# Optimization experiments

Hardware: AMD Instinct MI355X
Metric: run time of the kernel (lower is better)

The kernel has to match this reference:

```python
import jax, jax.numpy as jnp
import numpy as np

N = 100_000      # nodes
E = 800_000      # edges (avg degree 8)
IN = 64          # in_channels
OUT = 64         # out_channels
HEADS = 4
HD = OUT // HEADS  # per-head out channels (concat=True)


def _unif(key, shape, fan_in):
    b = 1.0 / np.sqrt(fan_in)
    return jax.random.uniform(key, shape, jnp.float32, -b, b)


def setup_inputs() -> dict:
    key = jax.random.key(0)
    ks = jax.random.split(key, 12)
    x = jax.random.normal(ks[0], (N, IN), jnp.float32)
    pos = jax.random.normal(ks[1], (N, 3), jnp.float32)
    edge_index = jax.random.randint(ks[2], (2, E), 0, N, jnp.int32)
    # Per-head PointTransformerConv params (stacked over heads).
    # lin / lin_src / lin_dst are bias-free Linear(in, hd); pos_nn is Linear(3, hd) with bias.
    W_lin = _unif(ks[3], (HEADS, IN, HD), IN)
    W_src = _unif(ks[4], (HEADS, IN, HD), IN)
    W_dst = _unif(ks[5], (HEADS, IN, HD), IN)
    W_pos = _unif(ks[6], (HEADS, 3, HD), 3)
    b_pos = _unif(ks[7], (HEADS, HD), 3)
    # projection MLP: Linear(OUT,OUT) -> ReLU -> Linear(OUT,OUT)
    W1 = _unif(ks[8], (OUT, OUT), OUT)
    b1 = _unif(ks[9], (OUT,), OUT)
    W2 = _unif(ks[10], (OUT, OUT), OUT)
    b2 = _unif(ks[11], (OUT,), OUT)
    return dict(x=x, pos=pos, edge_index=edge_index, W_lin=W_lin, W_src=W_src,
                W_dst=W_dst, W_pos=W_pos, b_pos=b_pos, W1=W1, b1=b1, W2=W2, b2=b2)


def reference(x, pos, edge_index, W_lin, W_src, W_dst, W_pos, b_pos, W1, b1, W2, b2):
    # Add self-loops (PointTransformerConv default add_self_loops=True).
    loops = jnp.arange(N, dtype=edge_index.dtype)
    src = jnp.concatenate([edge_index[0], loops])   # j (source)
    dst = jnp.concatenate([edge_index[1], loops])   # i (target)

    # Per-node, all-heads projections: [N, H, HD]
    v = jnp.einsum('ni,hio->nho', x, W_lin)
    a_src = jnp.einsum('ni,hio->nho', x, W_src)
    a_dst = jnp.einsum('ni,hio->nho', x, W_dst)

    # Relative-position encoding delta = pos_nn(pos_i - pos_j): [Et, H, HD]
    rel = pos[dst] - pos[src]
    delta = jnp.einsum('ec,hco->eho', rel, W_pos) + b_pos

    # Attention logits per edge/channel: alpha_i - alpha_j + delta
    alpha = a_dst[dst] - a_src[src] + delta

    # Segment softmax over incoming edges of each target node (numerically stable).
    amax = jax.ops.segment_max(alpha, dst, num_segments=N)
    amax = jnp.where(jnp.isfinite(amax), amax, 0.0)
    ex = jnp.exp(alpha - amax[dst])
    denom = jax.ops.segment_sum(ex, dst, num_segments=N)
    attn = ex / jnp.maximum(denom[dst], 1e-16)

    # Message = attn * (lin(x_j) + delta), scatter-sum to targets: [N, H, HD]
    msg = attn * (v[src] + delta)
    out_h = jax.ops.segment_sum(msg, dst, num_segments=N)

    # Concat heads -> projection MLP
    out = out_h.reshape(N, HEADS * HD)
    h = jax.nn.relu(out @ W1 + b1)
    return h @ W2 + b2
```

## Files before the change

### kernel.cpp

```cpp
#include <hip/hip_runtime.h>
#include <math.h>


typedef _Float16 f16;
typedef _Float16 f16x2 __attribute__((ext_vector_type(2)));
typedef _Float16 f16x4 __attribute__((ext_vector_type(4)));
typedef _Float16 f16x8 __attribute__((ext_vector_type(8)));
typedef float f32x4 __attribute__((ext_vector_type(4)));

#define A_PITCH 104
#define C_PITCH 200
#define LOG2E 1.44269504f
#define S_CAP 32

__global__ __launch_bounds__(256) void zero_wprep_kernel(
    int Zb, int* __restrict__ cnt, int N,
    const float* __restrict__ Ws, const float* __restrict__ Wl,
    const float* __restrict__ Wp, const float* __restrict__ bp,
    const float* __restrict__ W1, const float* __restrict__ W2,
    f16* __restrict__ Bt, f16* __restrict__ W1p, f16* __restrict__ W2p)
{
    if ((int)blockIdx.x < Zb) {
        int i4 = (blockIdx.x * 256 + threadIdx.x) * 4;
        if (i4 + 3 < N) {
            *(int4*)&cnt[i4] = make_int4(0, 0, 0, 0);
        } else {
            for (int i = i4; i < N; i++) cnt[i] = 0;
        }
        return;
    }
    int idx = (blockIdx.x - Zb) * 256 + threadIdx.x;
    if (idx < 192 * 96) {
        int col = idx / 96, k = idx - col * 96;
        float v = 0.f;
        if (col < 128) {
            int p = col >> 1, h = p >> 4, o = p & 15;
            if (col & 1) {
                if (k < 64)      v = Wl[h * 1024 + k * 16 + o];
                else if (k < 67) v = -Wp[h * 48 + (k - 64) * 16 + o];
            } else {
                if (k < 64)      v = -LOG2E * Ws[h * 1024 + k * 16 + o];
                else if (k < 67) v = -LOG2E * Wp[h * 48 + (k - 64) * 16 + o];
            }
        } else {
            int c = col - 128, h = c >> 4, o = c & 15;
            if (k >= 64 && k < 67) v = Wp[h * 48 + (k - 64) * 16 + o];
            else if (k == 67)      v = bp[c];
        }
        Bt[col * 96 + k] = (f16)v;
    } else if (idx < 192 * 96 + 4096) {
        int t = idx - 192 * 96;
        int col = t >> 6, k = t & 63;
        W1p[col * 64 + k] = (f16)W1[k * 64 + col];
    } else if (idx < 192 * 96 + 8192) {
        int t = idx - 192 * 96 - 4096;
        int col = t >> 6, k = t & 63;
        W2p[col * 64 + k] = (f16)W2[k * 64 + col];
    }
}

__global__ __launch_bounds__(256) void gemm_hist_kernel(
    const float* __restrict__ x, const float* __restrict__ pos,
    const f16* __restrict__ Bt,
    f16* __restrict__ AV, f16* __restrict__ G, int N, int Gb,
    const int* __restrict__ ei, int E, int Hb2,
    int* __restrict__ cnt, int* __restrict__ ssrc)
{
    __shared__ f16 smem[64 * C_PITCH];
    int tid = threadIdx.x;

    if (blockIdx.x & 1) {
        int hb = blockIdx.x >> 1;
        if (hb >= Hb2) return;
        int e0 = hb * 512 + tid;
        int e1 = e0 + 256;
        int s0 = 0, d0 = 0, s1 = 0, d1 = 0;
        bool a0 = e0 < E, a1 = e1 < E;
        if (a0) { s0 = ei[e0]; d0 = ei[E + e0]; }
        if (a1) { s1 = ei[e1]; d1 = ei[E + e1]; }
        if (a0) {
            int r = atomicAdd(&cnt[d0], 1);
            if (r < S_CAP) ssrc[d0 * S_CAP + r] = s0;
        }
        if (a1) {
            int r = atomicAdd(&cnt[d1], 1);
            if (r < S_CAP) ssrc[d1 * S_CAP + r] = s1;
        }
        return;
    }

    int gb = blockIdx.x >> 1;
    if (gb >= Gb) return;
    int l = tid & 63, wv = tid >> 6;
    int quad = l >> 4, lr = l & 15;
    int nb = gb * 64;

    for (int it = 0; it < 4; it++) {
        int q = it * 256 + tid;
        int n = q >> 4, k = (q & 15) * 4;
        float4 xv = make_float4(0.f, 0.f, 0.f, 0.f);
        if (nb + n < N) xv = *(const float4*)&x[(size_t)(nb + n) * 64 + k];
        f16x4 h4; h4[0] = (f16)xv.x; h4[1] = (f16)xv.y; h4[2] = (f16)xv.z; h4[3] = (f16)xv.w;
        *(f16x4*)&smem[n * A_PITCH + k] = h4;
    }
    {
        int n = tid >> 2, seg = tid & 3;
        f16x4 z = {(f16)0, (f16)0, (f16)0, (f16)0};
        f16x4 h4 = z;
        if (seg == 0 && nb + n < N) {
            h4[0] = (f16)pos[(size_t)(nb + n) * 3 + 0];
            h4[1] = (f16)pos[(size_t)(nb + n) * 3 + 1];
            h4[2] = (f16)pos[(size_t)(nb + n) * 3 + 2];
            h4[3] = (f16)1.0f;
        }
        *(f16x4*)&smem[n * A_PITCH + 64 + seg * 8] = h4;
        *(f16x4*)&smem[n * A_PITCH + 64 + seg * 8 + 4] = z;
    }
    __syncthreads();

    f16x8 af[4][3];
    #pragma unroll
    for (int mt = 0; mt < 4; mt++)
        #pragma unroll
        for (int kt = 0; kt < 3; kt++)
            af[mt][kt] = *(const f16x8*)&smem[(mt * 16 + lr) * A_PITCH + kt * 32 + quad * 8];
    __syncthreads();

    #pragma unroll
    for (int t = 0; t < 3; t++) {
        int colBase = (wv * 3 + t) * 16;
        f16x8 b0 = *(const f16x8*)&Bt[(colBase + lr) * 96 + 0  + quad * 8];
        f16x8 b1 = *(const f16x8*)&Bt[(colBase + lr) * 96 + 32 + quad * 8];
        f16x8 b2 = *(const f16x8*)&Bt[(colBase + lr) * 96 + 64 + quad * 8];
        #pragma unroll
        for (int mt = 0; mt < 4; mt++) {
            f32x4 acc = {0.f, 0.f, 0.f, 0.f};
            acc = __builtin_amdgcn_mfma_f32_16x16x32_f16(af[mt][0], b0, acc, 0, 0, 0);
            acc = __builtin_amdgcn_mfma_f32_16x16x32_f16(af[mt][1], b1, acc, 0, 0, 0);
            acc = __builtin_amdgcn_mfma_f32_16x16x32_f16(af[mt][2], b2, acc, 0, 0, 0);
            int col = colBase + lr;
            #pragma unroll
            for (int r = 0; r < 4; r++) {
                int row = mt * 16 + quad * 4 + r;
                smem[row * C_PITCH + col] = (f16)acc[r];
            }
        }
    }
    __syncthreads();

    for (int it = 0; it < 4; it++) {
        int cid = it * 256 + tid;
        int row = cid >> 4, off = (cid & 15) * 8;
        if (nb + row < N) {
            f16x8 w8 = *(const f16x8*)&smem[row * C_PITCH + off];
            f16x8 o;
            #pragma unroll
            for (int p = 0; p < 4; p++) {
                float e  = __builtin_amdgcn_exp2f((float)w8[2 * p]);
                float ev = e * (float)w8[2 * p + 1];
                o[2 * p]     = (f16)e;
                o[2 * p + 1] = (f16)ev;
            }
            *(f16x8*)&AV[(size_t)(nb + row) * 128 + off] = o;
        }
    }
    for (int it = 0; it < 2; it++) {
        int cid = it * 256 + tid;
        int row = cid >> 3, off = (cid & 7) * 8;
        if (nb + row < N)
            *(f16x8*)&G[(size_t)(nb + row) * 64 + off] =
                *(const f16x8*)&smem[row * C_PITCH + 128 + off];
    }
}

__global__ __launch_bounds__(256) void attn_mlp_kernel(
    const f16* __restrict__ AV, const f16* __restrict__ G,
    const int* __restrict__ cnt, const int* __restrict__ ssrc,
    const f16* __restrict__ W1p, const f16* __restrict__ W2p,
    const float* __restrict__ b1, const float* __restrict__ b2,
    float* __restrict__ out, int N)
{
    __shared__ f16 As[32 * 72];
    __shared__ f16 Hs[32 * 72];
    int tid = threadIdx.x, c = tid & 63, wv = tid >> 6;
    int quad = c >> 4, lr = c & 15;
    int nb = blockIdx.x * 32;

    const f16x2* AV2 = (const f16x2*)AV;

    for (int pt = 0; pt < 4; pt++) {
        int i0 = __builtin_amdgcn_readfirstlane(nb + wv * 8 + pt * 2);
        int i1 = i0 + 1;
        if (i1 >= N) i1 = N - 1;
        if (i0 >= N) i0 = N - 1;
        int deg0 = __builtin_amdgcn_readfirstlane(cnt[i0]); if (deg0 > S_CAP) deg0 = S_CAP;
        int deg1 = __builtin_amdgcn_readfirstlane(cnt[i1]); if (deg1 > S_CAP) deg1 = S_CAP;
        float Gi0 = (float)G[(size_t)i0 * 64 + c];
        float Gi1 = (float)G[(size_t)i1 * 64 + c];
        f16x2 sv0 = AV2[(size_t)i0 * 64 + c];
        f16x2 sv1 = AV2[(size_t)i1 * 64 + c];
        float den0 = (float)sv0[0], num0 = (float)sv0[1];
        float den1 = (float)sv1[0], num1 = (float)sv1[1];
        int base0 = i0 * S_CAP, base1 = i1 * S_CAP;

        for (int b = 0; b < S_CAP; b += 8) {
            bool r0 = b < deg0, r1 = b < deg1;
            if (!(r0 | r1)) break;
            f16x2 w0[8], w1[8];
            if (r0) {
                #pragma unroll
                for (int s = 0; s < 8; s++) {
                    int jj = __builtin_amdgcn_readfirstlane(ssrc[base0 + b + s]);
                    if ((unsigned)jj >= (unsigned)N) jj = 0;
                    w0[s] = AV2[(size_t)jj * 64 + c];
                }
            }
            if (r1) {
                #pragma unroll
                for (int s = 0; s < 8; s++) {
                    int jj = __builtin_amdgcn_readfirstlane(ssrc[base1 + b + s]);
                    if ((unsigned)jj >= (unsigned)N) jj = 0;
                    w1[s] = AV2[(size_t)jj * 64 + c];
                }
            }
            if (r0) {
                #pragma unroll
                for (int s = 0; s < 8; s++) {
                    bool ok = (b + s) < deg0;
                    den0 += ok ? (float)w0[s][0] : 0.f;
                    num0 += ok ? (float)w0[s][1] : 0.f;
                }
            }
            if (r1) {
                #pragma unroll
                for (int s = 0; s < 8; s++) {
                    bool ok = (b + s) < deg1;
                    den1 += ok ? (float)w1[s][0] : 0.f;
                    num1 += ok ? (float)w1[s][1] : 0.f;
                }
            }
        }
        As[(wv * 8 + pt * 2) * 72 + c]     = (f16)(num0 / den0 + Gi0);
        As[(wv * 8 + pt * 2 + 1) * 72 + c] = (f16)(num1 / den1 + Gi1);
    }
    __syncthreads();

    f16x8 af[2][2];
    #pragma unroll
    for (int mt = 0; mt < 2; mt++)
        #pragma unroll
        for (int kt = 0; kt < 2; kt++)
            af[mt][kt] = *(const f16x8*)&As[(mt * 16 + lr) * 72 + kt * 32 + quad * 8];

    int col = wv * 16 + lr;
    f16x8 wb0 = *(const f16x8*)&W1p[col * 64 + quad * 8];
    f16x8 wb1 = *(const f16x8*)&W1p[col * 64 + 32 + quad * 8];
    float bias1 = b1[col];
    #pragma unroll
    for (int mt = 0; mt < 2; mt++) {
        f32x4 acc = {0.f, 0.f, 0.f, 0.f};
        acc = __builtin_amdgcn_mfma_f32_16x16x32_f16(af[mt][0], wb0, acc, 0, 0, 0);
        acc = __builtin_amdgcn_mfma_f32_16x16x32_f16(af[mt][1], wb1, acc, 0, 0, 0);
        #pragma unroll
        for (int r = 0; r < 4; r++) {
            int row = mt * 16 + quad * 4 + r;
            Hs[row * 72 + col] = (f16)fmaxf(acc[r] + bias1, 0.f);
        }
    }
    __syncthreads();

    f16x8 ag[2][2];
    #pragma unroll
    for (int mt = 0; mt < 2; mt++)
        #pragma unroll
        for (int kt = 0; kt < 2; kt++)
            ag[mt][kt] = *(const f16x8*)&Hs[(mt * 16 + lr) * 72 + kt * 32 + quad * 8];

    f16x8 wc0 = *(const f16x8*)&W2p[col * 64 + quad * 8];
    f16x8 wc1 = *(const f16x8*)&W2p[col * 64 + 32 + quad * 8];
    float bias2 = b2[col];
    #pragma unroll
    for (int mt = 0; mt < 2; mt++) {
        f32x4 acc = {0.f, 0.f, 0.f, 0.f};
        acc = __builtin_amdgcn_mfma_f32_16x16x32_f16(ag[mt][0], wc0, acc, 0, 0, 0);
        acc = __builtin_amdgcn_mfma_f32_16x16x32_f16(ag[mt][1], wc1, acc, 0, 0, 0);
        #pragma unroll
        for (int r = 0; r < 4; r++) {
            int row = nb + mt * 16 + quad * 4 + r;
            if (row < N) out[(size_t)row * 64 + col] = acc[r] + bias2;
        }
    }
}

extern "C" void kernel_launch(void* const* d_in, const int* in_sizes, int n_in,
                              void* d_out, int out_size, void* d_ws, size_t ws_size,
                              hipStream_t stream)
{
    const float* x    = (const float*)d_in[0];
    const float* pos  = (const float*)d_in[1];
    const int*   ei   = (const int*)d_in[2];
    const float* Wl   = (const float*)d_in[3];
    const float* Ws   = (const float*)d_in[4];
    const float* Wp   = (const float*)d_in[6];
    const float* bpos = (const float*)d_in[7];
    const float* W1   = (const float*)d_in[8];
    const float* b1   = (const float*)d_in[9];
    const float* W2   = (const float*)d_in[10];
    const float* b2   = (const float*)d_in[11];
    float* out = (float*)d_out;

    const int N = in_sizes[0] / 64;
    const int E = in_sizes[2] / 2;

    char* w = (char*)d_ws;
    f16*  AV   = (f16*)w;                   w += (size_t)N * 128 * 2;
    f16*  G    = (f16*)w;                   w += (size_t)N * 64 * 2;
    f16*  Bt   = (f16*)w;                   w += 192 * 96 * 2;
    f16*  W1p  = (f16*)w;                   w += 4096 * 2;
    f16*  W2p  = (f16*)w;                   w += 4096 * 2;
    int*  cnt  = (int*)w;                   w += (size_t)N * 4;
    int*  ssrc = (int*)w;                   w += (size_t)N * S_CAP * 4;

    const int Zb  = (N + 1023) / 1024;
    const int Pb  = (192 * 96 + 8192 + 255) / 256;
    const int Gb  = (N + 63) / 64;
    const int Hb2 = (E + 511) / 512;
    const int Kb  = (Gb > Hb2 ? Gb : Hb2) * 2;

    zero_wprep_kernel<<<Zb + Pb, 256, 0, stream>>>(Zb, cnt, N, Ws, Wl, Wp, bpos,
                                                   W1, W2, Bt, W1p, W2p);
    gemm_hist_kernel<<<Kb, 256, 0, stream>>>(x, pos, Bt, AV, G, N, Gb,
                                             ei, E, Hb2, cnt, ssrc);
    attn_mlp_kernel<<<(N + 31) / 32, 256, 0, stream>>>(AV, G, cnt, ssrc, W1p, W2p,
                                                       b1, b2, out, N);
}
```

Baseline: 179.2 us.

## Recompute per-node position encoding in attention kernel; partition histogram by destination class

The G buffer (pos_nn of the target node) is no longer produced by the GEMM and written to global memory. The attention kernel now recomputes it from pos and Wp with three FMAs per lane. This shrinks the GEMM to 128 output columns and removes an N×64 f16 write and read. The edge histogram is split into four blocks per edge chunk, each handling the destinations in one residue class mod 4, which adds redundant reads of the destination indices in exchange for something about atomic or ssrc write locality. The gather loop also clamps out-of-degree slots to index 0 so that garbage source indices are never used.

```diff
diff --git a/kernel.cpp b/kernel.cpp
--- a/kernel.cpp
+++ b/kernel.cpp
@@ -9,14 +9,14 @@
 typedef float f32x4 __attribute__((ext_vector_type(4)));
 
 #define A_PITCH 104
-#define C_PITCH 200
+#define C_PITCH 136
 #define LOG2E 1.44269504f
 #define S_CAP 32
 
 __global__ __launch_bounds__(256) void zero_wprep_kernel(
     int Zb, int* __restrict__ cnt, int N,
     const float* __restrict__ Ws, const float* __restrict__ Wl,
-    const float* __restrict__ Wp, const float* __restrict__ bp,
+    const float* __restrict__ Wp,
     const float* __restrict__ W1, const float* __restrict__ W2,
     f16* __restrict__ Bt, f16* __restrict__ W1p, f16* __restrict__ W2p)
 {
@@ -30,30 +30,24 @@
         return;
     }
     int idx = (blockIdx.x - Zb) * 256 + threadIdx.x;
-    if (idx < 192 * 96) {
+    if (idx < 128 * 96) {
         int col = idx / 96, k = idx - col * 96;
         float v = 0.f;
-        if (col < 128) {
-            int p = col >> 1, h = p >> 4, o = p & 15;
-            if (col & 1) {
-                if (k < 64)      v = Wl[h * 1024 + k * 16 + o];
-                else if (k < 67) v = -Wp[h * 48 + (k - 64) * 16 + o];
-            } else {
-                if (k < 64)      v = -LOG2E * Ws[h * 1024 + k * 16 + o];
-                else if (k < 67) v = -LOG2E * Wp[h * 48 + (k - 64) * 16 + o];
-            }
+        int p = col >> 1, h = p >> 4, o = p & 15;
+        if (col & 1) {
+            if (k < 64)      v = Wl[h * 1024 + k * 16 + o];
+            else if (k < 67) v = -Wp[h * 48 + (k - 64) * 16 + o];
         } else {
-            int c = col - 128, h = c >> 4, o = c & 15;
-            if (k >= 64 && k < 67) v = Wp[h * 48 + (k - 64) * 16 + o];
-            else if (k == 67)      v = bp[c];
+            if (k < 64)      v = -LOG2E * Ws[h * 1024 + k * 16 + o];
+            else if (k < 67) v = -LOG2E * Wp[h * 48 + (k - 64) * 16 + o];
         }
         Bt[col * 96 + k] = (f16)v;
-    } else if (idx < 192 * 96 + 4096) {
-        int t = idx - 192 * 96;
+    } else if (idx < 128 * 96 + 4096) {
+        int t = idx - 128 * 96;
         int col = t >> 6, k = t & 63;
         W1p[col * 64 + k] = (f16)W1[k * 64 + col];
-    } else if (idx < 192 * 96 + 8192) {
-        int t = idx - 192 * 96 - 4096;
+    } else if (idx < 128 * 96 + 8192) {
+        int t = idx - 128 * 96 - 4096;
         int col = t >> 6, k = t & 63;
         W2p[col * 64 + k] = (f16)W2[k * 64 + col];
     }
@@ -62,8 +56,8 @@
 __global__ __launch_bounds__(256) void gemm_hist_kernel(
     const float* __restrict__ x, const float* __restrict__ pos,
     const f16* __restrict__ Bt,
-    f16* __restrict__ AV, f16* __restrict__ G, int N, int Gb,
-    const int* __restrict__ ei, int E, int Hb2,
+    f16* __restrict__ AV, int N, int Gb,
+    const int* __restrict__ ei, int E, int Hb4,
     int* __restrict__ cnt, int* __restrict__ ssrc)
 {
     __shared__ f16 smem[64 * C_PITCH];
@@ -71,18 +65,24 @@
 
     if (blockIdx.x & 1) {
         int hb = blockIdx.x >> 1;
-        if (hb >= Hb2) return;
-        int e0 = hb * 512 + tid;
+        if (hb >= Hb4) return;
+        int chunk = hb >> 2, cls = hb & 3;
+        int e0 = chunk * 512 + tid;
         int e1 = e0 + 256;
-        int s0 = 0, d0 = 0, s1 = 0, d1 = 0;
+        int d0 = 0, d1 = 0;
         bool a0 = e0 < E, a1 = e1 < E;
-        if (a0) { s0 = ei[e0]; d0 = ei[E + e0]; }
-        if (a1) { s1 = ei[e1]; d1 = ei[E + e1]; }
-        if (a0) {
+        if (a0) d0 = ei[E + e0];
+        if (a1) d1 = ei[E + e1];
+        bool k0 = a0 && ((d0 & 3) == cls);
+        bool k1 = a1 && ((d1 & 3) == cls);
+        int s0 = 0, s1 = 0;
+        if (k0) s0 = ei[e0];
+        if (k1) s1 = ei[e1];
+        if (k0) {
             int r = atomicAdd(&cnt[d0], 1);
             if (r < S_CAP) ssrc[d0 * S_CAP + r] = s0;
         }
-        if (a1) {
+        if (k1) {
             int r = atomicAdd(&cnt[d1], 1);
             if (r < S_CAP) ssrc[d1 * S_CAP + r] = s1;
         }
@@ -127,8 +127,8 @@
     __syncthreads();
 
     #pragma unroll
-    for (int t = 0; t < 3; t++) {
-        int colBase = (wv * 3 + t) * 16;
+    for (int t = 0; t < 2; t++) {
+        int colBase = (wv * 2 + t) * 16;
         f16x8 b0 = *(const f16x8*)&Bt[(colBase + lr) * 96 + 0  + quad * 8];
         f16x8 b1 = *(const f16x8*)&Bt[(colBase + lr) * 96 + 32 + quad * 8];
         f16x8 b2 = *(const f16x8*)&Bt[(colBase + lr) * 96 + 64 + quad * 8];
@@ -164,18 +164,13 @@
             *(f16x8*)&AV[(size_t)(nb + row) * 128 + off] = o;
         }
     }
-    for (int it = 0; it < 2; it++) {
-        int cid = it * 256 + tid;
-        int row = cid >> 3, off = (cid & 7) * 8;
-        if (nb + row < N)
-            *(f16x8*)&G[(size_t)(nb + row) * 64 + off] =
-                *(const f16x8*)&smem[row * C_PITCH + 128 + off];
-    }
 }
 
 __global__ __launch_bounds__(256) void attn_mlp_kernel(
-    const f16* __restrict__ AV, const f16* __restrict__ G,
+    const f16* __restrict__ AV,
     const int* __restrict__ cnt, const int* __restrict__ ssrc,
+    const float* __restrict__ pos, const float* __restrict__ Wp,
+    const float* __restrict__ bp,
     const f16* __restrict__ W1p, const f16* __restrict__ W2p,
     const float* __restrict__ b1, const float* __restrict__ b2,
     float* __restrict__ out, int N)
@@ -186,6 +181,11 @@
     int quad = c >> 4, lr = c & 15;
     int nb = blockIdx.x * 32;
 
+    float wpx = Wp[quad * 48 + 0  + lr];
+    float wpy = Wp[quad * 48 + 16 + lr];
+    float wpz = Wp[quad * 48 + 32 + lr];
+    float bpc = bp[c];
+
     const f16x2* AV2 = (const f16x2*)AV;
 
     for (int pt = 0; pt < 4; pt++) {
@@ -195,8 +195,8 @@
         if (i0 >= N) i0 = N - 1;
         int deg0 = __builtin_amdgcn_readfirstlane(cnt[i0]); if (deg0 > S_CAP) deg0 = S_CAP;
         int deg1 = __builtin_amdgcn_readfirstlane(cnt[i1]); if (deg1 > S_CAP) deg1 = S_CAP;
-        float Gi0 = (float)G[(size_t)i0 * 64 + c];
-        float Gi1 = (float)G[(size_t)i1 * 64 + c];
+        float Gi0 = pos[i0 * 3 + 0] * wpx + pos[i0 * 3 + 1] * wpy + pos[i0 * 3 + 2] * wpz + bpc;
+        float Gi1 = pos[i1 * 3 + 0] * wpx + pos[i1 * 3 + 1] * wpy + pos[i1 * 3 + 2] * wpz + bpc;
         f16x2 sv0 = AV2[(size_t)i0 * 64 + c];
         f16x2 sv1 = AV2[(size_t)i1 * 64 + c];
         float den0 = (float)sv0[0], num0 = (float)sv0[1];
@@ -211,7 +211,7 @@
                 #pragma unroll
                 for (int s = 0; s < 8; s++) {
                     int jj = __builtin_amdgcn_readfirstlane(ssrc[base0 + b + s]);
-                    if ((unsigned)jj >= (unsigned)N) jj = 0;
+                    if ((b + s) >= deg0 || (unsigned)jj >= (unsigned)N) jj = 0;
                     w0[s] = AV2[(size_t)jj * 64 + c];
                 }
             }
@@ -219,7 +219,7 @@
                 #pragma unroll
                 for (int s = 0; s < 8; s++) {
                     int jj = __builtin_amdgcn_readfirstlane(ssrc[base1 + b + s]);
-                    if ((unsigned)jj >= (unsigned)N) jj = 0;
+                    if ((b + s) >= deg1 || (unsigned)jj >= (unsigned)N) jj = 0;
                     w1[s] = AV2[(size_t)jj * 64 + c];
                 }
             }
@@ -314,23 +314,22 @@
 
     char* w = (char*)d_ws;
     f16*  AV   = (f16*)w;                   w += (size_t)N * 128 * 2;
-    f16*  G    = (f16*)w;                   w += (size_t)N * 64 * 2;
-    f16*  Bt   = (f16*)w;                   w += 192 * 96 * 2;
+    f16*  Bt   = (f16*)w;                   w += 128 * 96 * 2;
     f16*  W1p  = (f16*)w;                   w += 4096 * 2;
     f16*  W2p  = (f16*)w;                   w += 4096 * 2;
     int*  cnt  = (int*)w;                   w += (size_t)N * 4;
     int*  ssrc = (int*)w;                   w += (size_t)N * S_CAP * 4;
 
     const int Zb  = (N + 1023) / 1024;
-    const int Pb  = (192 * 96 + 8192 + 255) / 256;
+    const int Pb  = (128 * 96 + 8192 + 255) / 256;
     const int Gb  = (N + 63) / 64;
-    const int Hb2 = (E + 511) / 512;
-    const int Kb  = (Gb > Hb2 ? Gb : Hb2) * 2;
-
-    zero_wprep_kernel<<<Zb + Pb, 256, 0, stream>>>(Zb, cnt, N, Ws, Wl, Wp, bpos,
+    const int Hb4 = ((E + 511) / 512) * 4;
+    const int Kb  = (Gb > Hb4 ? Gb : Hb4) * 2;
+
+    zero_wprep_kernel<<<Zb + Pb, 256, 0, stream>>>(Zb, cnt, N, Ws, Wl, Wp,
                                                    W1, W2, Bt, W1p, W2p);
-    gemm_hist_kernel<<<Kb, 256, 0, stream>>>(x, pos, Bt, AV, G, N, Gb,
-                                             ei, E, Hb2, cnt, ssrc);
-    attn_mlp_kernel<<<(N + 31) / 32, 256, 0, stream>>>(AV, G, cnt, ssrc, W1p, W2p,
-                                                       b1, b2, out, N);
+    gemm_hist_kernel<<<Kb, 256, 0, stream>>>(x, pos, Bt, AV, N, Gb,
+                                             ei, E, Hb4, cnt, ssrc);
+    attn_mlp_kernel<<<(N + 31) / 32, 256, 0, stream>>>(AV, cnt, ssrc, pos, Wp, bpos,
+                                                       W1p, W2p, b1, b2, out, N);
 }
```

Measured after the change: 184.6 us. 3.0% more time.
